# Kernel optimization log

Hardware: AMD Instinct MI355X
Metric: run time of the kernel (lower is better)

Reference implementation:

```python
import jax, jax.numpy as jnp
import numpy as np

BS, N, H, F_IN, F_OUT = 4, 2048, 2, 768, 768
NEG_SLOPE = 0.2

def setup_inputs() -> dict:
    key = jax.random.key(0)
    k_h, k_adj, k_w, k_as, k_ad = jax.random.split(key, 5)
    h = jax.random.normal(k_h, (BS, N, F_IN), dtype=jnp.float32)
    adj = jax.random.randint(k_adj, (BS, N, N), 0, 2) > 0  # bool adjacency
    # xavier_uniform fan_in/fan_out per torch semantics on [H, f_in, f_out]
    limit_w = float(np.sqrt(6.0 / (F_IN + F_OUT)))
    w = jax.random.uniform(k_w, (H, F_IN, F_OUT), minval=-limit_w, maxval=limit_w, dtype=jnp.float32)
    limit_a = float(np.sqrt(6.0 / (F_OUT + 1)))
    a_src = jax.random.uniform(k_as, (H, F_OUT, 1), minval=-limit_a, maxval=limit_a, dtype=jnp.float32)
    a_dst = jax.random.uniform(k_ad, (H, F_OUT, 1), minval=-limit_a, maxval=limit_a, dtype=jnp.float32)
    bias = jnp.zeros((F_OUT,), dtype=jnp.float32)
    return {"h": h, "adj": adj, "w": w, "a_src": a_src, "a_dst": a_dst, "bias": bias}

def reference(h, adj, w, a_src, a_dst, bias):
    # h: [b, n, f_in]; w: [H, f_in, f_out] -> h_prime: [b, H, n, f_out]
    h_prime = jnp.einsum('bnf,hfo->bhno', h, w)
    t = jnp.tanh(h_prime)
    attn_src = jnp.einsum('bhno,ho->bhn', t, a_src[..., 0])  # [b, H, n]
    attn_dst = jnp.einsum('bhno,ho->bhn', t, a_dst[..., 0])  # [b, H, n]
    # broadcast add: scores[b,h,i,j] = src[i] + dst[j]
    attn = attn_src[:, :, :, None] + attn_dst[:, :, None, :]
    attn = jnp.where(attn >= 0, attn, NEG_SLOPE * attn)  # leaky_relu
    n = adj.shape[-1]
    keep = adj[:, None, :, :] | jnp.eye(n, dtype=bool)[None, None]  # [b,1,n,n]
    attn = jnp.where(keep, attn, -jnp.inf)
    attn = jax.nn.softmax(attn, axis=-1)
    # dropout is identity at inference
    out = jnp.einsum('bhij,bhjo->bhio', attn, h_prime)
    return out + bias
```

## Files before the change

kernel.cpp:

```cpp
#include <hip/hip_runtime.h>
#include <hip/hip_bf16.h>
#include <cstdint>
#include <cstddef>

#define BS   4
#define NN   2048
#define NH   2
#define FIN  768
#define FOUT 768
#define NEG_SLOPE 0.2f

typedef __attribute__((ext_vector_type(8))) short short8;
typedef __attribute__((ext_vector_type(4))) float float4v;

static __device__ __forceinline__ float bits2f(unsigned short u) {
    union { unsigned int i; float f; } v; v.i = ((unsigned int)u) << 16; return v.f;
}
static __device__ __forceinline__ unsigned short f2bits(float f) {
    union { float f; unsigned int i; } v; v.f = f;
    unsigned int x = v.i;
    unsigned int r = x + 0x7fffu + ((x >> 16) & 1u);
    return (unsigned short)(r >> 16);
}
static __device__ __forceinline__ float fast_tanh(float x) {
    float xc = fminf(fmaxf(x, -20.f), 20.f);
    float e = __expf(2.f * xc);
    return (e - 1.f) / (e + 1.f);
}
static __device__ __forceinline__ void async_copy16(void* lds, const void* g) {
    __builtin_amdgcn_global_load_lds(
        (const __attribute__((address_space(1))) unsigned int*)g,
        (__attribute__((address_space(3))) unsigned int*)lds, 16, 0, 0);
}

static __device__ __forceinline__ bool detect_isf32(const unsigned short* h_raw) {
    unsigned short u = h_raw[threadIdx.x & 63];
    int e = (u >> 7) & 0xFF;
    unsigned long long m = __ballot(e >= 118 && e <= 134);
    return __popcll(m) < 48;
}
static __device__ __forceinline__ bool detect_adj8(const unsigned char* adj_raw) {
    int l = threadIdx.x & 63;
    unsigned char v = (unsigned char)(adj_raw[l * 4 + 1] | adj_raw[l * 4 + 2] |
                                      adj_raw[l * 4 + 3]);
    unsigned long long m = __ballot(v != 0);
    return __popcll(m) > 8;
}

#define NB_H   3072
#define NB_W   1152
#define NB_Z   128
__global__ __launch_bounds__(256) void k_prep(
    const void* __restrict__ hr, unsigned short* __restrict__ h_bf,
    const void* __restrict__ wr, unsigned short* __restrict__ wt_b,
    const void* __restrict__ as_raw, const void* __restrict__ ad_raw,
    const void* __restrict__ b_raw,
    float* __restrict__ asf, float* __restrict__ adf, float* __restrict__ bff,
    float* __restrict__ attn_acc)
{
    __shared__ float tile[32][33];
    int bi = blockIdx.x;
    int t = threadIdx.x;
    if (bi < NB_H) {
        bool isf = detect_isf32((const unsigned short*)hr);
        int base = (bi * 256 + t) * 8;
        if (isf) {
            float4 f0 = *((const float4*)((const float*)hr + base));
            float4 f1 = *((const float4*)((const float*)hr + base + 4));
            unsigned short v[8] = { f2bits(f0.x), f2bits(f0.y), f2bits(f0.z), f2bits(f0.w),
                                    f2bits(f1.x), f2bits(f1.y), f2bits(f1.z), f2bits(f1.w) };
            *(uint4*)(h_bf + base) = *(const uint4*)v;
        } else {
            *(uint4*)(h_bf + base) = *(const uint4*)((const unsigned short*)hr + base);
        }
        return;
    }
    if (bi < NB_H + NB_W) {
        bool isf = detect_isf32((const unsigned short*)hr);
        int wb = bi - NB_H;
        int h  = wb / 576;
        int rem = wb % 576;
        int f0 = (rem % 24) * 32;
        int o0 = (rem / 24) * 32;
        int tx = t & 31, ty = t >> 5;
        #pragma unroll
        for (int r = 0; r < 4; ++r) {
            int fl = ty * 4 + r;
            size_t idx = (size_t)h * FIN * FOUT + (size_t)(f0 + fl) * FOUT + (o0 + tx);
            tile[fl][tx] = isf ? ((const float*)wr)[idx]
                               : bits2f(((const unsigned short*)wr)[idx]);
        }
        __syncthreads();
        #pragma unroll
        for (int r = 0; r < 4; ++r) {
            int ol = ty * 4 + r;
            size_t oidx = (size_t)h * FOUT * FIN + (size_t)(o0 + ol) * FIN + (f0 + tx);
            wt_b[oidx] = f2bits(tile[tx][ol]);
        }
        return;
    }
    if (bi < NB_H + NB_W + NB_Z) {
        attn_acc[(bi - NB_H - NB_W) * 256 + t] = 0.f;
        return;
    }
    bool isf = detect_isf32((const unsigned short*)hr);
    for (int i = t; i < NH * FOUT; i += 256) {
        asf[i] = isf ? ((const float*)as_raw)[i] : bits2f(((const unsigned short*)as_raw)[i]);
        adf[i] = isf ? ((const float*)ad_raw)[i] : bits2f(((const unsigned short*)ad_raw)[i]);
    }
    for (int i = t; i < FOUT; i += 256)
        bff[i] = isf ? ((const float*)b_raw)[i] : bits2f(((const unsigned short*)b_raw)[i]);
}

#define BM 128
#define BN 128
#define BK 64
#define NXB (NN / BM)
#define NYB (FOUT / BN)
#define BLKS_PER_BATCH (NXB * NYB)
#define GEMM_GRID (BLKS_PER_BATCH * BS * NH)

__global__ __launch_bounds__(256) void k_gemm_hw(
    const unsigned short* __restrict__ hh,
    const unsigned short* __restrict__ wh,
    unsigned short* __restrict__ hpT,
    const float* __restrict__ asf, const float* __restrict__ adf,
    float* __restrict__ attn_src, float* __restrict__ attn_dst)
{
    int lid = blockIdx.x;
    int ib  = lid & 7;
    int rem = lid >> 3;
    int i0  = (rem & 15) * BM;
    int o0  = (rem >> 4) * BN;
    int b  = ib / NH, hd = ib % NH;
    const unsigned short* A  = hh + (size_t)b  * NN * FIN;
    const unsigned short* Bt = wh + (size_t)hd * FOUT * FIN;
    unsigned short*       C  = hpT + (size_t)ib * FOUT * NN;

    __shared__ __align__(16) unsigned short As[BM * BK];
    __shared__ __align__(16) unsigned short Bs[BN * BK];

    int t = threadIdx.x;
    int lane = t & 63, wave = t >> 6;
    int wm = (wave & 1) * 64, wn = (wave >> 1) * 64;
    int lm = lane & 15, quad = lane >> 4;
    int rr = lane >> 3;
    int cc = lane & 7;
    int gc = cc ^ rr;
    int e  = lm & 7;

    float4v acc[4][4] = {};

    for (int k0 = 0; k0 < FIN; k0 += BK) {
        __syncthreads();
        #pragma unroll
        for (int p = 0; p < 4; ++p) {
            int r0 = wave * 32 + p * 8;
            async_copy16(&As[r0 * BK], A  + (size_t)(i0 + r0 + rr) * FIN + k0 + gc * 8);
            async_copy16(&Bs[r0 * BK], Bt + (size_t)(o0 + r0 + rr) * FIN + k0 + gc * 8);
        }
        __syncthreads();
        #pragma unroll
        for (int kk = 0; kk < 2; ++kk) {
            int slot = ((kk << 2) | quad) ^ e;
            short8 fa[4], fb[4];
            #pragma unroll
            for (int mt = 0; mt < 4; ++mt)
                fa[mt] = *(const short8*)&As[(wm + mt * 16 + lm) * BK + slot * 8];
            #pragma unroll
            for (int nt = 0; nt < 4; ++nt)
                fb[nt] = *(const short8*)&Bs[(wn + nt * 16 + lm) * BK + slot * 8];
            #pragma unroll
            for (int mt = 0; mt < 4; ++mt)
                #pragma unroll
                for (int nt = 0; nt < 4; ++nt)
                    acc[mt][nt] = __builtin_amdgcn_mfma_f32_16x16x32_bf16(
                        fa[mt], fb[nt], acc[mt][nt], 0, 0, 0);
        }
    }

    float asv[4], adv[4];
    #pragma unroll
    for (int nt = 0; nt < 4; ++nt) {
        int o = o0 + wn + nt * 16 + lm;
        asv[nt] = asf[hd * FOUT + o];
        adv[nt] = adf[hd * FOUT + o];
    }
    #pragma unroll
    for (int mt = 0; mt < 4; ++mt) {
        float ps[4] = {0.f, 0.f, 0.f, 0.f};
        float pd[4] = {0.f, 0.f, 0.f, 0.f};
        #pragma unroll
        for (int nt = 0; nt < 4; ++nt) {
            int node = i0 + wm + mt * 16 + quad * 4;
            int o    = o0 + wn + nt * 16 + lm;
            ushort4 v;
            v.x = f2bits(acc[mt][nt][0]);
            v.y = f2bits(acc[mt][nt][1]);
            v.z = f2bits(acc[mt][nt][2]);
            v.w = f2bits(acc[mt][nt][3]);
            *(ushort4*)&C[(size_t)o * NN + node] = v;
            #pragma unroll
            for (int r = 0; r < 4; ++r) {
                float tv = fast_tanh(acc[mt][nt][r]);
                ps[r] += tv * asv[nt];
                pd[r] += tv * adv[nt];
            }
        }
        #pragma unroll
        for (int r = 0; r < 4; ++r) {
            float s = ps[r], d = pd[r];
            #pragma unroll
            for (int off = 1; off <= 8; off <<= 1) {
                s += __shfl_xor(s, off);
                d += __shfl_xor(d, off);
            }
            if (lm == 0) {
                int node = i0 + wm + mt * 16 + quad * 4 + r;
                atomicAdd(&attn_src[ib * NN + node], s);
                atomicAdd(&attn_dst[ib * NN + node], d);
            }
        }
    }
}

__global__ __launch_bounds__(256) void k_softmax_p(
    const float* __restrict__ attn_src, const float* __restrict__ attn_dst,
    const void* __restrict__ adj_raw,
    unsigned short* __restrict__ P)
{
    int blk = blockIdx.x;
    int i = blk & (NN - 1);
    int b = blk >> 11;
    bool is8 = detect_adj8((const unsigned char*)adj_raw);
    int t = threadIdx.x;
    int lane = t & 63, wave = t >> 6;
    int j0 = t * 8;

    bool keep[8];
    if (is8) {
        const unsigned char* arow = (const unsigned char*)adj_raw + ((size_t)b * NN + i) * NN;
        uint2 v = *(const uint2*)(arow + j0);
        #pragma unroll
        for (int r = 0; r < 8; ++r) {
            unsigned int w = (r < 4) ? v.x : v.y;
            keep[r] = ((w >> ((r & 3) * 8)) & 0xFFu) != 0;
        }
    } else {
        const int* arow = (const int*)adj_raw + ((size_t)b * NN + i) * NN;
        int4 v0 = *(const int4*)(arow + j0);
        int4 v1 = *(const int4*)(arow + j0 + 4);
        keep[0] = v0.x != 0; keep[1] = v0.y != 0; keep[2] = v0.z != 0; keep[3] = v0.w != 0;
        keep[4] = v1.x != 0; keep[5] = v1.y != 0; keep[6] = v1.z != 0; keep[7] = v1.w != 0;
    }
    #pragma unroll
    for (int r = 0; r < 8; ++r) keep[r] = keep[r] || (j0 + r == i);

    __shared__ float redm[NH][4], reds[NH][4];
    int bh0 = b * NH;
    float src0 = attn_src[(size_t)bh0 * NN + i];
    float src1 = attn_src[(size_t)(bh0 + 1) * NN + i];
    const float* drow0 = attn_dst + (size_t)bh0 * NN;
    const float* drow1 = attn_dst + (size_t)(bh0 + 1) * NN;
    float4 a0 = *(const float4*)(drow0 + j0);
    float4 a1 = *(const float4*)(drow0 + j0 + 4);
    float4 c0 = *(const float4*)(drow1 + j0);
    float4 c1 = *(const float4*)(drow1 + j0 + 4);
    float dj0[8] = { a0.x, a0.y, a0.z, a0.w, a1.x, a1.y, a1.z, a1.w };
    float dj1[8] = { c0.x, c0.y, c0.z, c0.w, c1.x, c1.y, c1.z, c1.w };

    float s0[8], s1[8];
    float lm0 = -1e30f, lm1 = -1e30f;
    #pragma unroll
    for (int r = 0; r < 8; ++r) {
        float sc0 = src0 + dj0[r];
        sc0 = sc0 >= 0.f ? sc0 : NEG_SLOPE * sc0;
        s0[r] = keep[r] ? sc0 : -1e30f;
        lm0 = fmaxf(lm0, s0[r]);
        float sc1 = src1 + dj1[r];
        sc1 = sc1 >= 0.f ? sc1 : NEG_SLOPE * sc1;
        s1[r] = keep[r] ? sc1 : -1e30f;
        lm1 = fmaxf(lm1, s1[r]);
    }
    #pragma unroll
    for (int off = 32; off > 0; off >>= 1) {
        lm0 = fmaxf(lm0, __shfl_xor(lm0, off));
        lm1 = fmaxf(lm1, __shfl_xor(lm1, off));
    }
    if (lane == 0) { redm[0][wave] = lm0; redm[1][wave] = lm1; }
    __syncthreads();
    float m0 = fmaxf(fmaxf(redm[0][0], redm[0][1]), fmaxf(redm[0][2], redm[0][3]));
    float m1 = fmaxf(fmaxf(redm[1][0], redm[1][1]), fmaxf(redm[1][2], redm[1][3]));

    float p0[8], p1[8];
    float ls0 = 0.f, ls1 = 0.f;
    #pragma unroll
    for (int r = 0; r < 8; ++r) {
        p0[r] = __expf(s0[r] - m0); ls0 += p0[r];
        p1[r] = __expf(s1[r] - m1); ls1 += p1[r];
    }
    #pragma unroll
    for (int off = 32; off > 0; off >>= 1) {
        ls0 += __shfl_xor(ls0, off);
        ls1 += __shfl_xor(ls1, off);
    }
    if (lane == 0) { reds[0][wave] = ls0; reds[1][wave] = ls1; }
    __syncthreads();
    float inv0 = 1.0f / (reds[0][0] + reds[0][1] + reds[0][2] + reds[0][3]);
    float inv1 = 1.0f / (reds[1][0] + reds[1][1] + reds[1][2] + reds[1][3]);

    uint4 pw;
    pw.x = ((unsigned int)f2bits(p0[1] * inv0) << 16) | f2bits(p0[0] * inv0);
    pw.y = ((unsigned int)f2bits(p0[3] * inv0) << 16) | f2bits(p0[2] * inv0);
    pw.z = ((unsigned int)f2bits(p0[5] * inv0) << 16) | f2bits(p0[4] * inv0);
    pw.w = ((unsigned int)f2bits(p0[7] * inv0) << 16) | f2bits(p0[6] * inv0);
    *(uint4*)&P[((size_t)bh0 * NN + i) * NN + j0] = pw;
    pw.x = ((unsigned int)f2bits(p1[1] * inv1) << 16) | f2bits(p1[0] * inv1);
    pw.y = ((unsigned int)f2bits(p1[3] * inv1) << 16) | f2bits(p1[2] * inv1);
    pw.z = ((unsigned int)f2bits(p1[5] * inv1) << 16) | f2bits(p1[4] * inv1);
    pw.w = ((unsigned int)f2bits(p1[7] * inv1) << 16) | f2bits(p1[6] * inv1);
    *(uint4*)&P[((size_t)(bh0 + 1) * NN + i) * NN + j0] = pw;
}

#define BM2 256
#define BN2 192
#define BK2 64
#define NT2 (NN / BK2)
#define GRID2 (8 * (NN / BM2) * (FOUT / BN2))

__global__ __launch_bounds__(1024, 4) void k_gemm_out(
    const unsigned short* __restrict__ P,
    const unsigned short* __restrict__ hpT,
    const float* __restrict__ bf,
    void* __restrict__ outp, const unsigned short* __restrict__ h_raw)
{
    bool isf = detect_isf32(h_raw);
    int lid = blockIdx.x;
    int ib  = lid & 7;
    int rem = lid >> 3;
    int i0  = (rem & 7) * BM2;
    int o0  = (rem >> 3) * BN2;
    const unsigned short* A  = P   + (size_t)ib * NN * NN;
    const unsigned short* Bt = hpT + (size_t)ib * FOUT * NN;

    __shared__ __align__(16) unsigned short As[3][BM2 * BK2];
    __shared__ __align__(16) unsigned short Bs[2][BN2 * BK2];

    int t = threadIdx.x;
    int lane = t & 63, wave = t >> 6;
    int wr = wave >> 2, wc = wave & 3;
    int wm = wr * 64, wn = wc * 48;
    int lm = lane & 15, quad = lane >> 4;
    int e  = lm & 7;
    int rr = lane >> 3, cc = lane & 7, gc = cc ^ rr;
    bool prod = (wave < 8);

    float4v acc[4][3] = {};

    auto stageA = [&](int slot, int q, int kt) {
        int r0 = q * 64 + wave * 8;
        async_copy16(&As[slot][r0 * BK2],
                     A + (size_t)(i0 + r0 + rr) * NN + kt * BK2 + gc * 8);
    };
    auto stageB = [&](int slot, int q, int kt) {
        int r0 = q * 64 + wave * 8;
        async_copy16(&Bs[slot][r0 * BK2],
                     Bt + (size_t)(o0 + r0 + rr) * NN + kt * BK2 + gc * 8);
    };

    if (prod) {
        stageA(0, 0, 0); stageA(0, 1, 0); stageA(0, 2, 0); stageA(0, 3, 0);
        stageB(0, 0, 0); stageB(0, 1, 0); stageB(0, 2, 0);
        stageA(1, 0, 1); stageA(1, 1, 1); stageA(1, 2, 1); stageA(1, 3, 1);
    }
    asm volatile("s_waitcnt vmcnt(4)" ::: "memory");
    __builtin_amdgcn_s_barrier();

    short8 fa[2][2];
    short8 fb[3][2];

    int sr = 0;
    for (int u = 0; u < NT2; ++u) {
        int sw = sr + 2; if (sw >= 3) sw -= 3;
        int sbw = (u + 1) & 1;
        bool moreA = (u < NT2 - 2);
        bool moreB = (u < NT2 - 1);
        const unsigned short* Ac = As[sr];
        const unsigned short* Bc = Bs[u & 1];

        #pragma unroll
        for (int nt = 0; nt < 3; ++nt)
            #pragma unroll
            for (int kk = 0; kk < 2; ++kk)
                fb[nt][kk] = *(const short8*)&Bc[(wn + nt * 16 + lm) * BK2 +
                                                 ((((kk << 2) | quad) ^ e) * 8)];
        #pragma unroll
        for (int mt = 0; mt < 2; ++mt)
            #pragma unroll
            for (int kk = 0; kk < 2; ++kk)
                fa[mt][kk] = *(const short8*)&Ac[(wm + mt * 16 + lm) * BK2 +
                                                 ((((kk << 2) | quad) ^ e) * 8)];
        if (prod && moreB) { stageB(sbw, 0, u + 1); stageB(sbw, 1, u + 1);
                             stageB(sbw, 2, u + 1); }
        if (prod && moreA) { stageA(sw, 0, u + 2); stageA(sw, 1, u + 2); }
        __builtin_amdgcn_s_barrier();
        __builtin_amdgcn_s_setprio(1);
        #pragma unroll
        for (int mt = 0; mt < 2; ++mt)
            #pragma unroll
            for (int nt = 0; nt < 3; ++nt)
                #pragma unroll
                for (int kk = 0; kk < 2; ++kk)
                    acc[mt][nt] = __builtin_amdgcn_mfma_f32_16x16x32_bf16(
                        fa[mt][kk], fb[nt][kk], acc[mt][nt], 0, 0, 0);
        __builtin_amdgcn_s_setprio(0);
        __builtin_amdgcn_s_barrier();

        #pragma unroll
        for (int mt = 0; mt < 2; ++mt)
            #pragma unroll
            for (int kk = 0; kk < 2; ++kk)
                fa[mt][kk] = *(const short8*)&Ac[(wm + 32 + mt * 16 + lm) * BK2 +
                                                 ((((kk << 2) | quad) ^ e) * 8)];
        if (prod && moreA) { stageA(sw, 2, u + 2); stageA(sw, 3, u + 2); }
        __builtin_amdgcn_s_barrier();
        __builtin_amdgcn_s_setprio(1);
        #pragma unroll
        for (int mt = 0; mt < 2; ++mt)
            #pragma unroll
            for (int nt = 0; nt < 3; ++nt)
                #pragma unroll
                for (int kk = 0; kk < 2; ++kk)
                    acc[2 + mt][nt] = __builtin_amdgcn_mfma_f32_16x16x32_bf16(
                        fa[mt][kk], fb[nt][kk], acc[2 + mt][nt], 0, 0, 0);
        __builtin_amdgcn_s_setprio(0);
        if (moreA)      asm volatile("s_waitcnt vmcnt(4)" ::: "memory");
        else if (moreB) asm volatile("s_waitcnt vmcnt(0)" ::: "memory");
        __builtin_amdgcn_s_barrier();

        sr = sr + 1 == 3 ? 0 : sr + 1;
    }

    if (isf) {
        float* C = (float*)outp + (size_t)ib * NN * FOUT;
        #pragma unroll
        for (int nt = 0; nt < 3; ++nt) {
            int o = o0 + wn + nt * 16 + lm;
            float bv = bf[o];
            #pragma unroll
            for (int mt = 0; mt < 4; ++mt) {
                int i = i0 + wm + mt * 16 + quad * 4;
                #pragma unroll
                for (int r = 0; r < 4; ++r)
                    C[(size_t)(i + r) * FOUT + o] = acc[mt][nt][r] + bv;
            }
        }
    } else {
        unsigned short* C = (unsigned short*)outp + (size_t)ib * NN * FOUT;
        #pragma unroll
        for (int nt = 0; nt < 3; ++nt) {
            int o = o0 + wn + nt * 16 + lm;
            float bv = bf[o];
            #pragma unroll
            for (int mt = 0; mt < 4; ++mt) {
                int i = i0 + wm + mt * 16 + quad * 4;
                #pragma unroll
                for (int r = 0; r < 4; ++r)
                    C[(size_t)(i + r) * FOUT + o] = f2bits(acc[mt][nt][r] + bv);
            }
        }
    }
}

extern "C" void kernel_launch(void* const* d_in, const int* in_sizes, int n_in,
                              void* d_out, int out_size, void* d_ws, size_t ws_size,
                              hipStream_t stream)
{
    const void* h_raw   = d_in[0];
    const void* adj_raw = d_in[1];
    const void* w_raw   = d_in[2];
    const void* as_raw  = d_in[3];
    const void* ad_raw  = d_in[4];
    const void* b_raw   = d_in[5];

    char* ws = (char*)d_ws;
    size_t off = 0;
    unsigned short* hpT = (unsigned short*)(ws + off); off += (size_t)BS * NH * FOUT * NN * 2;
    float* asr = (float*)(ws + off);            off += (size_t)BS * NH * NN * 4;
    float* ads = (float*)(ws + off);            off += (size_t)BS * NH * NN * 4;
    size_t uoff = off;
    unsigned short* P    = (unsigned short*)(ws + uoff);
    unsigned short* h_bf = (unsigned short*)(ws + uoff); uoff += (size_t)BS * NN * FIN * 2;
    unsigned short* wt_b = (unsigned short*)(ws + uoff); uoff += (size_t)NH * FOUT * FIN * 2;
    off += (size_t)BS * NH * NN * NN * 2;
    float* asf = (float*)(ws + off);            off += (size_t)NH * FOUT * 4;
    float* adf = (float*)(ws + off);            off += (size_t)NH * FOUT * 4;
    float* bff = (float*)(ws + off);            off += 4096;

    k_prep<<<NB_H + NB_W + NB_Z + 1, 256, 0, stream>>>(
        h_raw, h_bf, w_raw, wt_b, as_raw, ad_raw, b_raw, asf, adf, bff, asr);
    k_gemm_hw<<<dim3(GEMM_GRID), 256, 0, stream>>>(
        h_bf, wt_b, hpT, asf, adf, asr, ads);
    k_softmax_p<<<dim3(BS * NN), 256, 0, stream>>>(asr, ads, adj_raw, P);
    k_gemm_out<<<dim3(GRID2), 1024, 0, stream>>>(
        P, hpT, bff, d_out, (const unsigned short*)h_raw);
}
```

Measured before the change: 254.0 us.

## Fuse softmax probability generation into output GEMM A-tile staging

The softmax kernel now writes only per-row max and inverse sum. The output GEMM recomputes the bf16 attention probabilities for each A tile from attn_src, attn_dst and the adjacency mask, and writes them directly into shared memory. This drops the 64 MB P matrix write and its re-read. In exchange, exp work is repeated once for each of the four output column tiles, the A-tile staging drops from a triple buffer to a double buffer, and every iteration now waits for all loads to finish.

```diff
diff --git a/kernel.cpp b/kernel.cpp
--- a/kernel.cpp
+++ b/kernel.cpp
@@ -224,10 +224,10 @@
     }
 }
 
-__global__ __launch_bounds__(256) void k_softmax_p(
+__global__ __launch_bounds__(256) void k_softmax_stats(
     const float* __restrict__ attn_src, const float* __restrict__ attn_dst,
     const void* __restrict__ adj_raw,
-    unsigned short* __restrict__ P)
+    float2* __restrict__ minv)
 {
     int blk = blockIdx.x;
     int i = blk & (NN - 1);
@@ -292,12 +292,11 @@
     float m0 = fmaxf(fmaxf(redm[0][0], redm[0][1]), fmaxf(redm[0][2], redm[0][3]));
     float m1 = fmaxf(fmaxf(redm[1][0], redm[1][1]), fmaxf(redm[1][2], redm[1][3]));
 
-    float p0[8], p1[8];
     float ls0 = 0.f, ls1 = 0.f;
     #pragma unroll
     for (int r = 0; r < 8; ++r) {
-        p0[r] = __expf(s0[r] - m0); ls0 += p0[r];
-        p1[r] = __expf(s1[r] - m1); ls1 += p1[r];
+        ls0 += __expf(s0[r] - m0);
+        ls1 += __expf(s1[r] - m1);
     }
     #pragma unroll
     for (int off = 32; off > 0; off >>= 1) {
@@ -306,20 +305,12 @@
     }
     if (lane == 0) { reds[0][wave] = ls0; reds[1][wave] = ls1; }
     __syncthreads();
-    float inv0 = 1.0f / (reds[0][0] + reds[0][1] + reds[0][2] + reds[0][3]);
-    float inv1 = 1.0f / (reds[1][0] + reds[1][1] + reds[1][2] + reds[1][3]);
-
-    uint4 pw;
-    pw.x = ((unsigned int)f2bits(p0[1] * inv0) << 16) | f2bits(p0[0] * inv0);
-    pw.y = ((unsigned int)f2bits(p0[3] * inv0) << 16) | f2bits(p0[2] * inv0);
-    pw.z = ((unsigned int)f2bits(p0[5] * inv0) << 16) | f2bits(p0[4] * inv0);
-    pw.w = ((unsigned int)f2bits(p0[7] * inv0) << 16) | f2bits(p0[6] * inv0);
-    *(uint4*)&P[((size_t)bh0 * NN + i) * NN + j0] = pw;
-    pw.x = ((unsigned int)f2bits(p1[1] * inv1) << 16) | f2bits(p1[0] * inv1);
-    pw.y = ((unsigned int)f2bits(p1[3] * inv1) << 16) | f2bits(p1[2] * inv1);
-    pw.z = ((unsigned int)f2bits(p1[5] * inv1) << 16) | f2bits(p1[4] * inv1);
-    pw.w = ((unsigned int)f2bits(p1[7] * inv1) << 16) | f2bits(p1[6] * inv1);
-    *(uint4*)&P[((size_t)(bh0 + 1) * NN + i) * NN + j0] = pw;
+    if (t == 0) {
+        float inv0 = 1.0f / (reds[0][0] + reds[0][1] + reds[0][2] + reds[0][3]);
+        float inv1 = 1.0f / (reds[1][0] + reds[1][1] + reds[1][2] + reds[1][3]);
+        minv[(size_t)bh0 * NN + i]       = make_float2(m0, inv0);
+        minv[(size_t)(bh0 + 1) * NN + i] = make_float2(m1, inv1);
+    }
 }
 
 #define BM2 256
@@ -329,21 +320,25 @@
 #define GRID2 (8 * (NN / BM2) * (FOUT / BN2))
 
 __global__ __launch_bounds__(1024, 4) void k_gemm_out(
-    const unsigned short* __restrict__ P,
+    const float2* __restrict__ minv,
+    const float* __restrict__ attn_src, const float* __restrict__ attn_dst,
+    const void* __restrict__ adj_raw,
     const unsigned short* __restrict__ hpT,
     const float* __restrict__ bf,
     void* __restrict__ outp, const unsigned short* __restrict__ h_raw)
 {
     bool isf = detect_isf32(h_raw);
+    bool is8 = detect_adj8((const unsigned char*)adj_raw);
     int lid = blockIdx.x;
     int ib  = lid & 7;
     int rem = lid >> 3;
     int i0  = (rem & 7) * BM2;
     int o0  = (rem >> 3) * BN2;
-    const unsigned short* A  = P   + (size_t)ib * NN * NN;
+    int b   = ib / NH;
     const unsigned short* Bt = hpT + (size_t)ib * FOUT * NN;
-
-    __shared__ __align__(16) unsigned short As[3][BM2 * BK2];
+    const float* dstp = attn_dst + (size_t)ib * NN;
+
+    __shared__ __align__(16) unsigned short As[2][BM2 * BK2];
     __shared__ __align__(16) unsigned short Bs[2][BN2 * BK2];
 
     int t = threadIdx.x;
@@ -355,38 +350,110 @@
     int rr = lane >> 3, cc = lane & 7, gc = cc ^ rr;
     bool prod = (wave < 8);
 
+    int pr  = t >> 3;
+    int pcc = t & 7;
+    int pgc = pcc ^ (pr & 7);
+    int i1 = i0 + pr, i2 = i1 + 128;
+    float srcR1 = attn_src[(size_t)ib * NN + i1];
+    float srcR2 = attn_src[(size_t)ib * NN + i2];
+    float2 q1 = minv[(size_t)ib * NN + i1];
+    float2 q2 = minv[(size_t)ib * NN + i2];
+    int esz = is8 ? 1 : 4;
+    const char* ab1 = (const char*)adj_raw + ((size_t)b * NN + i1) * NN * esz;
+    const char* ab2 = (const char*)adj_raw + ((size_t)b * NN + i2) * NN * esz;
+
     float4v acc[4][3] = {};
 
-    auto stageA = [&](int slot, int q, int kt) {
-        int r0 = q * 64 + wave * 8;
-        async_copy16(&As[slot][r0 * BK2],
-                     A + (size_t)(i0 + r0 + rr) * NN + kt * BK2 + gc * 8);
-    };
     auto stageB = [&](int slot, int q, int kt) {
         int r0 = q * 64 + wave * 8;
         async_copy16(&Bs[slot][r0 * BK2],
                      Bt + (size_t)(o0 + r0 + rr) * NN + kt * BK2 + gc * 8);
     };
-
-    if (prod) {
-        stageA(0, 0, 0); stageA(0, 1, 0); stageA(0, 2, 0); stageA(0, 3, 0);
-        stageB(0, 0, 0); stageB(0, 1, 0); stageB(0, 2, 0);
-        stageA(1, 0, 1); stageA(1, 1, 1); stageA(1, 2, 1); stageA(1, 3, 1);
-    }
-    asm volatile("s_waitcnt vmcnt(4)" ::: "memory");
+    auto kmask8 = [](uint2 c) -> unsigned {
+        unsigned m = 0;
+        #pragma unroll
+        for (int r = 0; r < 8; ++r) {
+            unsigned w = (r < 4) ? c.x : c.y;
+            if ((w >> ((r & 3) * 8)) & 0xFFu) m |= 1u << r;
+        }
+        return m;
+    };
+    auto kmask32 = [](int4 a, int4 bq) -> unsigned {
+        return (unsigned)((a.x != 0)       | ((a.y != 0) << 1) |
+                          ((a.z != 0) << 2) | ((a.w != 0) << 3) |
+                          ((bq.x != 0) << 4) | ((bq.y != 0) << 5) |
+                          ((bq.z != 0) << 6) | ((bq.w != 0) << 7));
+    };
+    auto writeP = [&](unsigned short* dl, int j0n, float4 d0, float4 d1,
+                      unsigned kb1, unsigned kb2) {
+        float dj[8] = { d0.x, d0.y, d0.z, d0.w, d1.x, d1.y, d1.z, d1.w };
+        unsigned short o1[8], o2[8];
+        #pragma unroll
+        for (int r2 = 0; r2 < 8; ++r2) {
+            float s1 = srcR1 + dj[r2];
+            s1 = s1 >= 0.f ? s1 : NEG_SLOPE * s1;
+            bool k1 = ((kb1 >> r2) & 1u) || (j0n + r2 == i1);
+            o1[r2] = k1 ? f2bits(__expf(s1 - q1.x) * q1.y) : (unsigned short)0;
+            float s2 = srcR2 + dj[r2];
+            s2 = s2 >= 0.f ? s2 : NEG_SLOPE * s2;
+            bool k2 = ((kb2 >> r2) & 1u) || (j0n + r2 == i2);
+            o2[r2] = k2 ? f2bits(__expf(s2 - q2.x) * q2.y) : (unsigned short)0;
+        }
+        uint4 w1, w2;
+        w1.x = ((unsigned)o1[1] << 16) | o1[0]; w1.y = ((unsigned)o1[3] << 16) | o1[2];
+        w1.z = ((unsigned)o1[5] << 16) | o1[4]; w1.w = ((unsigned)o1[7] << 16) | o1[6];
+        w2.x = ((unsigned)o2[1] << 16) | o2[0]; w2.y = ((unsigned)o2[3] << 16) | o2[2];
+        w2.z = ((unsigned)o2[5] << 16) | o2[4]; w2.w = ((unsigned)o2[7] << 16) | o2[6];
+        *(uint4*)&dl[pr * BK2 + pcc * 8] = w1;
+        *(uint4*)&dl[(pr + 128) * BK2 + pcc * 8] = w2;
+    };
+
+    if (prod) { stageB(0, 0, 0); stageB(0, 1, 0); stageB(0, 2, 0); }
+    {
+        int j0n = pgc * 8;
+        float4 d0 = *(const float4*)(dstp + j0n);
+        float4 d1 = *(const float4*)(dstp + j0n + 4);
+        unsigned kb1, kb2;
+        if (is8) {
+            kb1 = kmask8(*(const uint2*)(ab1 + j0n));
+            kb2 = kmask8(*(const uint2*)(ab2 + j0n));
+        } else {
+            kb1 = kmask32(*(const int4*)(ab1 + 4 * j0n),
+                          *(const int4*)(ab1 + 4 * j0n + 16));
+            kb2 = kmask32(*(const int4*)(ab2 + 4 * j0n),
+                          *(const int4*)(ab2 + 4 * j0n + 16));
+        }
+        writeP(As[0], j0n, d0, d1, kb1, kb2);
+    }
+    asm volatile("s_waitcnt vmcnt(0) lgkmcnt(0)" ::: "memory");
     __builtin_amdgcn_s_barrier();
 
     short8 fa[2][2];
     short8 fb[3][2];
 
-    int sr = 0;
     for (int u = 0; u < NT2; ++u) {
-        int sw = sr + 2; if (sw >= 3) sw -= 3;
-        int sbw = (u + 1) & 1;
-        bool moreA = (u < NT2 - 2);
-        bool moreB = (u < NT2 - 1);
-        const unsigned short* Ac = As[sr];
-        const unsigned short* Bc = Bs[u & 1];
+        int cur = u & 1, nxt = cur ^ 1;
+        bool more = (u < NT2 - 1);
+        const unsigned short* Ac = As[cur];
+        const unsigned short* Bc = Bs[cur];
+        int j0n = (u + 1) * BK2 + pgc * 8;
+
+        float4 d0, d1; uint2 c1, c2; unsigned kb1 = 0, kb2 = 0;
+        if (more) {
+            d0 = *(const float4*)(dstp + j0n);
+            d1 = *(const float4*)(dstp + j0n + 4);
+            if (is8) {
+                c1 = *(const uint2*)(ab1 + j0n);
+                c2 = *(const uint2*)(ab2 + j0n);
+            } else {
+                kb1 = kmask32(*(const int4*)(ab1 + 4 * j0n),
+                              *(const int4*)(ab1 + 4 * j0n + 16));
+                kb2 = kmask32(*(const int4*)(ab2 + 4 * j0n),
+                              *(const int4*)(ab2 + 4 * j0n + 16));
+            }
+        }
+        if (prod && more) { stageB(nxt, 0, u + 1); stageB(nxt, 1, u + 1);
+                            stageB(nxt, 2, u + 1); }
 
         #pragma unroll
         for (int nt = 0; nt < 3; ++nt)
@@ -400,9 +467,6 @@
             for (int kk = 0; kk < 2; ++kk)
                 fa[mt][kk] = *(const short8*)&Ac[(wm + mt * 16 + lm) * BK2 +
                                                  ((((kk << 2) | quad) ^ e) * 8)];
-        if (prod && moreB) { stageB(sbw, 0, u + 1); stageB(sbw, 1, u + 1);
-                             stageB(sbw, 2, u + 1); }
-        if (prod && moreA) { stageA(sw, 0, u + 2); stageA(sw, 1, u + 2); }
         __builtin_amdgcn_s_barrier();
         __builtin_amdgcn_s_setprio(1);
         #pragma unroll
@@ -422,7 +486,6 @@
             for (int kk = 0; kk < 2; ++kk)
                 fa[mt][kk] = *(const short8*)&Ac[(wm + 32 + mt * 16 + lm) * BK2 +
                                                  ((((kk << 2) | quad) ^ e) * 8)];
-        if (prod && moreA) { stageA(sw, 2, u + 2); stageA(sw, 3, u + 2); }
         __builtin_amdgcn_s_barrier();
         __builtin_amdgcn_s_setprio(1);
         #pragma unroll
@@ -434,11 +497,12 @@
                     acc[2 + mt][nt] = __builtin_amdgcn_mfma_f32_16x16x32_bf16(
                         fa[mt][kk], fb[nt][kk], acc[2 + mt][nt], 0, 0, 0);
         __builtin_amdgcn_s_setprio(0);
-        if (moreA)      asm volatile("s_waitcnt vmcnt(4)" ::: "memory");
-        else if (moreB) asm volatile("s_waitcnt vmcnt(0)" ::: "memory");
+        if (more) {
+            if (is8) { kb1 = kmask8(c1); kb2 = kmask8(c2); }
+            writeP(As[nxt], j0n, d0, d1, kb1, kb2);
+        }
+        asm volatile("s_waitcnt vmcnt(0) lgkmcnt(0)" ::: "memory");
         __builtin_amdgcn_s_barrier();
-
-        sr = sr + 1 == 3 ? 0 : sr + 1;
     }
 
     if (isf) {
@@ -488,20 +552,18 @@
     unsigned short* hpT = (unsigned short*)(ws + off); off += (size_t)BS * NH * FOUT * NN * 2;
     float* asr = (float*)(ws + off);            off += (size_t)BS * NH * NN * 4;
     float* ads = (float*)(ws + off);            off += (size_t)BS * NH * NN * 4;
-    size_t uoff = off;
-    unsigned short* P    = (unsigned short*)(ws + uoff);
-    unsigned short* h_bf = (unsigned short*)(ws + uoff); uoff += (size_t)BS * NN * FIN * 2;
-    unsigned short* wt_b = (unsigned short*)(ws + uoff); uoff += (size_t)NH * FOUT * FIN * 2;
-    off += (size_t)BS * NH * NN * NN * 2;
+    unsigned short* h_bf = (unsigned short*)(ws + off); off += (size_t)BS * NN * FIN * 2;
+    unsigned short* wt_b = (unsigned short*)(ws + off); off += (size_t)NH * FOUT * FIN * 2;
     float* asf = (float*)(ws + off);            off += (size_t)NH * FOUT * 4;
     float* adf = (float*)(ws + off);            off += (size_t)NH * FOUT * 4;
     float* bff = (float*)(ws + off);            off += 4096;
+    float2* minv = (float2*)(ws + off);         off += (size_t)BS * NH * NN * 8;
 
     k_prep<<<NB_H + NB_W + NB_Z + 1, 256, 0, stream>>>(
         h_raw, h_bf, w_raw, wt_b, as_raw, ad_raw, b_raw, asf, adf, bff, asr);
     k_gemm_hw<<<dim3(GEMM_GRID), 256, 0, stream>>>(
         h_bf, wt_b, hpT, asf, adf, asr, ads);
-    k_softmax_p<<<dim3(BS * NN), 256, 0, stream>>>(asr, ads, adj_raw, P);
+    k_softmax_stats<<<dim3(BS * NN), 256, 0, stream>>>(asr, ads, adj_raw, minv);
     k_gemm_out<<<dim3(GRID2), 1024, 0, stream>>>(
-        P, hpT, bff, d_out, (const unsigned short*)h_raw);
-}
+        minv, asr, ads, adj_raw, hpT, bff, d_out, (const unsigned short*)h_raw);
+}
```

Measured after the change: 499.6 us. +96.7%, slower.
